# Kernel optimization log

Hardware: AMD Instinct MI355X
Metric: run time of the kernel (lower is better)

Reference implementation:

```python
import jax, jax.numpy as jnp
import numpy as np

N_NODES = 100000
N_EDGES = 3200000
IN_SIZE = 256
HID_SIZE = 256
OUT_SIZE = 64


def setup_inputs() -> dict:
    key = jax.random.key(0)
    ks = jax.random.split(key, 8)
    X = jax.random.normal(ks[0], (N_NODES, IN_SIZE), dtype=jnp.float32)
    edge_vals = jax.random.uniform(ks[1], (N_EDGES,), dtype=jnp.float32)
    # xavier-uniform-ish init for weights
    lim1 = float(np.sqrt(6.0 / (IN_SIZE + HID_SIZE)))
    W1 = jax.random.uniform(ks[2], (IN_SIZE, HID_SIZE), minval=-lim1, maxval=lim1, dtype=jnp.float32)
    b1 = jnp.zeros((HID_SIZE,), dtype=jnp.float32)
    lim2 = float(np.sqrt(6.0 / (HID_SIZE + OUT_SIZE)))
    W2 = jax.random.uniform(ks[3], (HID_SIZE, OUT_SIZE), minval=-lim2, maxval=lim2, dtype=jnp.float32)
    b2 = jnp.zeros((OUT_SIZE,), dtype=jnp.float32)
    row = jnp.sort(jax.random.randint(ks[4], (N_EDGES,), 0, N_NODES, dtype=jnp.int32))
    col = jax.random.randint(ks[5], (N_EDGES,), 0, N_NODES, dtype=jnp.int32)
    return {"X": X, "edge_vals": edge_vals, "W1": W1, "b1": b1,
            "W2": W2, "b2": b2, "row": row, "col": col}


def reference(X, edge_vals, W1, b1, W2, b2, row, col):
    """2-layer GCN (eval mode, dropout = identity).

    A is a sparse NxN matrix in COO form: A[row[e], col[e]] = edge_vals[e].
    Layer: relu(A @ (X @ W1) + b1); output: A @ (h @ W2) + b2.
    """
    n = X.shape[0]

    def spmm(dense):  # (A @ dense): gather columns, scale, segment-sum over rows
        gathered = edge_vals[:, None] * dense[col]        # [E, F]
        return jax.ops.segment_sum(gathered, row, num_segments=n)

    h = spmm(X @ W1) + b1          # [N, HID]
    h = jax.nn.relu(h)
    out = spmm(h @ W2) + b2        # [N, OUT]
    return out
```

## Files before the change

### kernel.cpp

```cpp
#include <hip/hip_runtime.h>


constexpr int IN_SIZE = 256;
constexpr int HID = 256;
constexpr int OUTF = 64;

typedef __bf16 bf16x8 __attribute__((ext_vector_type(8)));
typedef float f32x4 __attribute__((ext_vector_type(4)));

__device__ __forceinline__ ushort f2b(float f) {
    uint u = __float_as_uint(f);
    uint r = (u + 0x7fffu + ((u >> 16) & 1u)) >> 16;
    return (ushort)r;
}

__device__ __forceinline__ void fma4(float* a, uint word, float w) {
    a[0] += w * (float)(word & 0xffu);
    a[1] += w * (float)((word >> 8) & 0xffu);
    a[2] += w * (float)((word >> 16) & 0xffu);
    a[3] += w * (float)(word >> 24);
}

__device__ __forceinline__ bf16x8 pack8n(float4 a, float4 b) {
    bf16x8 h;
    h[0] = (__bf16)a.x; h[1] = (__bf16)a.y;
    h[2] = (__bf16)a.z; h[3] = (__bf16)a.w;
    h[4] = (__bf16)b.x; h[5] = (__bf16)b.y;
    h[6] = (__bf16)b.z; h[7] = (__bf16)b.w;
    return h;
}

__global__ void setup_kernel(const int* __restrict__ row, int* __restrict__ rp,
                             const float* __restrict__ W1, ushort* __restrict__ W1T,
                             const float* __restrict__ W2, ushort* __restrict__ W2T,
                             int n, int E, int rpB) {
    int b = blockIdx.x;
    if (b < rpB) {
        int i = b * 256 + threadIdx.x;
        if (i > n) return;
        int lo = 0, hi = E;
        while (lo < hi) {
            int mid = (lo + hi) >> 1;
            if (row[mid] < i) lo = mid + 1; else hi = mid;
        }
        rp[i] = lo;
    } else if (b < rpB + 256) {
        int nn = b - rpB;
        int k = threadIdx.x;
        W1T[(size_t)nn * 256 + k] = f2b(W1[(size_t)k * 256 + nn]);
    } else {
        int nn = b - rpB - 256;
        int k = threadIdx.x;
        W2T[(size_t)nn * 256 + k] = f2b(W2[(size_t)k * 64 + nn]);
    }
}

__global__ void prep_edges(const float* __restrict__ vals, const int* __restrict__ col,
                           const float* __restrict__ s, int2* __restrict__ ew,
                           int E, int shift) {
    int e = blockIdx.x * 256 + threadIdx.x;
    if (e >= E) return;
    int c = col[e];
    ew[e] = make_int2(c << shift, __float_as_int(vals[e] * s[c]));
}

__global__ __launch_bounds__(1024)
void gemm1_q(const float* __restrict__ A, const ushort* __restrict__ Bt,
             unsigned char* __restrict__ Q, float* __restrict__ s1, int M, int R) {
    __shared__ uint4 Wlds[8192];
    __shared__ float red[512];
    __shared__ float fin[256];
    const int tid = threadIdx.x;
    const int wave = tid >> 6, lane = tid & 63;
    const int quad = lane >> 4, l = lane & 15;
    const int wr = wave >> 1, wc = wave & 1;
    const int mstart = blockIdx.x * R;
    const int mend = min(mstart + R, M);

    for (int i = tid; i < 8192; i += 1024) {
        uint4 v = ((const uint4*)Bt)[i];
        Wlds[(i & ~31) | ((i & 31) ^ ((i >> 5) & 7))] = v;
    }
    __syncthreads();

    for (int m0 = mstart; m0 < mend; m0 += 256) {
        size_t abase[2];
#pragma unroll
        for (int mt = 0; mt < 2; ++mt) {
            int r = min(m0 + wr * 32 + mt * 16 + l, M - 1);
            abase[mt] = (size_t)r * 256 + quad * 8;
        }

        f32x4 acc[2][8] = {};
        float4 ra0[2], rb0[2], ra1[2], rb1[2];
#pragma unroll
        for (int mt = 0; mt < 2; ++mt) {
            ra0[mt] = *(const float4*)(A + abase[mt]);
            rb0[mt] = *(const float4*)(A + abase[mt] + 4);
            ra1[mt] = *(const float4*)(A + abase[mt] + 32);
            rb1[mt] = *(const float4*)(A + abase[mt] + 36);
        }

#pragma unroll
        for (int kstep = 0; kstep < 8; ++kstep) {
            bf16x8 af[2];
#pragma unroll
            for (int mt = 0; mt < 2; ++mt)
                af[mt] = pack8n(ra0[mt], rb0[mt]);
#pragma unroll
            for (int mt = 0; mt < 2; ++mt) { ra0[mt] = ra1[mt]; rb0[mt] = rb1[mt]; }
            if (kstep < 6) {
#pragma unroll
                for (int mt = 0; mt < 2; ++mt) {
                    ra1[mt] = *(const float4*)(A + abase[mt] + (kstep + 2) * 32);
                    rb1[mt] = *(const float4*)(A + abase[mt] + (kstep + 2) * 32 + 4);
                }
            }
#pragma unroll
            for (int nt = 0; nt < 8; ++nt) {
                int c = wc * 128 + nt * 16 + l;
                int idx = c * 32 + (((kstep << 2) + quad) ^ (c & 7));
                bf16x8 bfr = *(const bf16x8*)&Wlds[idx];
#pragma unroll
                for (int mt = 0; mt < 2; ++mt)
                    acc[mt][nt] = __builtin_amdgcn_mfma_f32_16x16x32_bf16(
                        af[mt], bfr, acc[mt][nt], 0, 0, 0);
            }
        }

        float rmax[2][4];
#pragma unroll
        for (int mt = 0; mt < 2; ++mt)
#pragma unroll
            for (int reg = 0; reg < 4; ++reg) {
                float m = 0.f;
#pragma unroll
                for (int nt = 0; nt < 8; ++nt)
                    m = fmaxf(m, fabsf(acc[mt][nt][reg]));
                rmax[mt][reg] = m;
            }
#pragma unroll
        for (int s = 1; s <= 8; s <<= 1)
#pragma unroll
            for (int mt = 0; mt < 2; ++mt)
#pragma unroll
                for (int reg = 0; reg < 4; ++reg)
                    rmax[mt][reg] = fmaxf(rmax[mt][reg], __shfl_xor(rmax[mt][reg], s));
        if (l < 4) {
#pragma unroll
            for (int mt = 0; mt < 2; ++mt)
                red[wc * 256 + wr * 32 + mt * 16 + quad * 4 + l] = rmax[mt][l];
        }
        __syncthreads();
        if (tid < 256) {
            float m = fmaxf(red[tid], red[256 + tid]);
            fin[tid] = m;
            int r = m0 + tid;
            if (r < mend) s1[r] = m * (1.f / 127.f);
        }
        __syncthreads();

#pragma unroll
        for (int mt = 0; mt < 2; ++mt)
#pragma unroll
            for (int reg = 0; reg < 4; ++reg) {
                int rl = wr * 32 + mt * 16 + quad * 4 + reg;
                int r = m0 + rl;
                if (r >= mend) continue;
                float m = fin[rl];
                float inv = m > 0.f ? 127.f / m : 0.f;
#pragma unroll
                for (int nt = 0; nt < 8; ++nt) {
                    int c = wc * 128 + nt * 16 + l;
                    Q[(size_t)r * 256 + c] =
                        (unsigned char)((int)rintf(acc[mt][nt][reg] * inv) + 128);
                }
            }
    }
}

__global__ __launch_bounds__(256, 4)
void gemm2_q(const ushort* __restrict__ A, const ushort* __restrict__ Bt,
             unsigned char* __restrict__ Q, float* __restrict__ s2, int M) {
    __shared__ uint4 Wlds[2048];
    const int tid = threadIdx.x;
    const int wave = tid >> 6, lane = tid & 63;
    const int quad = lane >> 4, l = lane & 15;
    const int r0 = blockIdx.x * 128 + wave * 32;

    for (int i = tid; i < 2048; i += 256) {
        uint4 v = ((const uint4*)Bt)[i];
        Wlds[(i & ~31) | ((i & 31) ^ ((i >> 5) & 7))] = v;
    }
    __syncthreads();

    size_t abase[2];
#pragma unroll
    for (int mt = 0; mt < 2; ++mt) {
        int r = min(r0 + mt * 16 + l, M - 1);
        abase[mt] = (size_t)r * 256 + quad * 8;
    }

    f32x4 acc[2][4] = {};
    uint4 ra0[2], ra1[2];
#pragma unroll
    for (int mt = 0; mt < 2; ++mt) {
        ra0[mt] = *(const uint4*)(A + abase[mt]);
        ra1[mt] = *(const uint4*)(A + abase[mt] + 32);
    }

#pragma unroll
    for (int kstep = 0; kstep < 8; ++kstep) {
        bf16x8 af[2];
#pragma unroll
        for (int mt = 0; mt < 2; ++mt)
            af[mt] = *(const bf16x8*)&ra0[mt];
#pragma unroll
        for (int mt = 0; mt < 2; ++mt) ra0[mt] = ra1[mt];
        if (kstep < 6) {
#pragma unroll
            for (int mt = 0; mt < 2; ++mt)
                ra1[mt] = *(const uint4*)(A + abase[mt] + (kstep + 2) * 32);
        }
        bf16x8 bfr[4];
#pragma unroll
        for (int nt = 0; nt < 4; ++nt) {
            int c = nt * 16 + l;
            int idx = c * 32 + (((kstep << 2) + quad) ^ (c & 7));
            bfr[nt] = *(const bf16x8*)&Wlds[idx];
        }
#pragma unroll
        for (int mt = 0; mt < 2; ++mt)
#pragma unroll
            for (int nt = 0; nt < 4; ++nt)
                acc[mt][nt] = __builtin_amdgcn_mfma_f32_16x16x32_bf16(
                    af[mt], bfr[nt], acc[mt][nt], 0, 0, 0);
    }

    float rmax[2][4];
#pragma unroll
    for (int mt = 0; mt < 2; ++mt)
#pragma unroll
        for (int reg = 0; reg < 4; ++reg) {
            float m = fmaxf(fabsf(acc[mt][0][reg]), fabsf(acc[mt][1][reg]));
            m = fmaxf(m, fabsf(acc[mt][2][reg]));
            m = fmaxf(m, fabsf(acc[mt][3][reg]));
            rmax[mt][reg] = m;
        }
#pragma unroll
    for (int s = 1; s <= 8; s <<= 1)
#pragma unroll
        for (int mt = 0; mt < 2; ++mt)
#pragma unroll
            for (int reg = 0; reg < 4; ++reg)
                rmax[mt][reg] = fmaxf(rmax[mt][reg], __shfl_xor(rmax[mt][reg], s));

#pragma unroll
    for (int mt = 0; mt < 2; ++mt)
#pragma unroll
        for (int reg = 0; reg < 4; ++reg) {
            int r = r0 + mt * 16 + quad * 4 + reg;
            if (r >= M) continue;
            float m = rmax[mt][reg];
            if (l == 0) s2[r] = m * (1.f / 127.f);
            float inv = m > 0.f ? 127.f / m : 0.f;
#pragma unroll
            for (int nt = 0; nt < 4; ++nt) {
                int c = nt * 16 + l;
                Q[(size_t)r * 64 + c] =
                    (unsigned char)((int)rintf(acc[mt][nt][reg] * inv) + 128);
            }
        }
}

__global__ __launch_bounds__(256)
void spmm1_q(const unsigned char* __restrict__ Q, const int2* __restrict__ ew,
             const int* __restrict__ rp, const float* __restrict__ bias,
             ushort* __restrict__ H, int node0, int nend) {
    const int wave = threadIdx.x >> 6;
    const int lane = threadIdx.x & 63;
    const int node = node0 + blockIdx.x * 4 + wave;
    if (node >= nend) return;
    const int e0 = rp[node], e1 = rp[node + 1];
    const int g = lane >> 4;
    const int fb = (lane & 15) * 16;

    float acc[16] = {};
    float sumw = 0.f;
    int e = e0;
    for (; e + 16 <= e1; e += 16) {
#pragma unroll
        for (int u = 0; u < 4; ++u) {
            int2 m = ew[e + u * 4 + g];
            float w = __int_as_float(m.y);
            uint4 qv = *(const uint4*)(Q + (size_t)(uint)m.x + fb);
            sumw += w;
            fma4(&acc[0], qv.x, w);
            fma4(&acc[4], qv.y, w);
            fma4(&acc[8], qv.z, w);
            fma4(&acc[12], qv.w, w);
        }
    }
    for (; e < e1; e += 4) {
        int idx = e + g;
        int2 m = ew[idx];
        bool ok = idx < e1;
        uint off = ok ? (uint)m.x : 0u;
        float w = ok ? __int_as_float(m.y) : 0.f;
        uint4 qv = *(const uint4*)(Q + (size_t)off + fb);
        sumw += w;
        fma4(&acc[0], qv.x, w);
        fma4(&acc[4], qv.y, w);
        fma4(&acc[8], qv.z, w);
        fma4(&acc[12], qv.w, w);
    }

#pragma unroll
    for (int s = 16; s <= 32; s <<= 1) {
#pragma unroll
        for (int j = 0; j < 16; ++j)
            acc[j] += __shfl_xor(acc[j], s);
        sumw += __shfl_xor(sumw, s);
    }

    if (g == 0) {
        const int f0 = (lane & 15) * 16;
        float4 b0 = *(const float4*)(bias + f0);
        float4 b1 = *(const float4*)(bias + f0 + 4);
        float4 b2 = *(const float4*)(bias + f0 + 8);
        float4 b3 = *(const float4*)(bias + f0 + 12);
        float bb[16] = {b0.x, b0.y, b0.z, b0.w, b1.x, b1.y, b1.z, b1.w,
                        b2.x, b2.y, b2.z, b2.w, b3.x, b3.y, b3.z, b3.w};
        float fix = -128.f * sumw;
        ushort r[16];
#pragma unroll
        for (int j = 0; j < 16; ++j)
            r[j] = f2b(fmaxf(acc[j] + fix + bb[j], 0.f));
        uint4 w0, w1;
        w0.x = (uint)r[0] | ((uint)r[1] << 16);
        w0.y = (uint)r[2] | ((uint)r[3] << 16);
        w0.z = (uint)r[4] | ((uint)r[5] << 16);
        w0.w = (uint)r[6] | ((uint)r[7] << 16);
        w1.x = (uint)r[8] | ((uint)r[9] << 16);
        w1.y = (uint)r[10] | ((uint)r[11] << 16);
        w1.z = (uint)r[12] | ((uint)r[13] << 16);
        w1.w = (uint)r[14] | ((uint)r[15] << 16);
        *(uint4*)(H + (size_t)node * 256 + f0) = w0;
        *(uint4*)(H + (size_t)node * 256 + f0 + 8) = w1;
    }
}

__global__ __launch_bounds__(256)
void spmm2_q(const unsigned char* __restrict__ Q, const int2* __restrict__ ew,
             const int* __restrict__ rp, const float* __restrict__ bias,
             float* __restrict__ O, int n) {
    const int wave = threadIdx.x >> 6;
    const int lane = threadIdx.x & 63;
    const int node = blockIdx.x * 4 + wave;
    if (node >= n) return;
    const int e0 = rp[node], e1 = rp[node + 1];
    const int g = lane >> 3;
    const int fb = (lane & 7) * 8;

    float acc[8] = {};
    float sumw = 0.f;
    int e = e0;
    for (; e + 16 <= e1; e += 16) {
#pragma unroll
        for (int u = 0; u < 2; ++u) {
            int2 m = ew[e + u * 8 + g];
            float w = __int_as_float(m.y);
            uint2 qv = *(const uint2*)(Q + (size_t)(uint)m.x + fb);
            sumw += w;
            fma4(&acc[0], qv.x, w);
            fma4(&acc[4], qv.y, w);
        }
    }
    for (; e < e1; e += 8) {
        int idx = e + g;
        int2 m = ew[idx];
        bool ok = idx < e1;
        uint off = ok ? (uint)m.x : 0u;
        float w = ok ? __int_as_float(m.y) : 0.f;
        uint2 qv = *(const uint2*)(Q + (size_t)off + fb);
        sumw += w;
        fma4(&acc[0], qv.x, w);
        fma4(&acc[4], qv.y, w);
    }

#pragma unroll
    for (int s = 8; s <= 32; s <<= 1) {
#pragma unroll
        for (int j = 0; j < 8; ++j)
            acc[j] += __shfl_xor(acc[j], s);
        sumw += __shfl_xor(sumw, s);
    }

    if (g == 0) {
        const int f0 = (lane & 7) * 8;
        float4 b0 = *(const float4*)(bias + f0);
        float4 b1 = *(const float4*)(bias + f0 + 4);
        float fix = -128.f * sumw;
        float4 o0, o1;
        o0.x = acc[0] + fix + b0.x;
        o0.y = acc[1] + fix + b0.y;
        o0.z = acc[2] + fix + b0.z;
        o0.w = acc[3] + fix + b0.w;
        o1.x = acc[4] + fix + b1.x;
        o1.y = acc[5] + fix + b1.y;
        o1.z = acc[6] + fix + b1.z;
        o1.w = acc[7] + fix + b1.w;
        *(float4*)(O + (size_t)node * 64 + f0) = o0;
        *(float4*)(O + (size_t)node * 64 + f0 + 4) = o1;
    }
}

static inline size_t alignup(size_t x) { return (x + 255) & ~(size_t)255; }

extern "C" void kernel_launch(void* const* d_in, const int* in_sizes, int n_in,
                              void* d_out, int out_size, void* d_ws, size_t ws_size,
                              hipStream_t stream) {
    const float* X  = (const float*)d_in[0];
    const float* ev = (const float*)d_in[1];
    const float* W1 = (const float*)d_in[2];
    const float* b1 = (const float*)d_in[3];
    const float* W2 = (const float*)d_in[4];
    const float* b2 = (const float*)d_in[5];
    const int*  row = (const int*)d_in[6];
    const int*  col = (const int*)d_in[7];
    float* out = (float*)d_out;

    const int n = in_sizes[0] / IN_SIZE;
    const int E = in_sizes[1];

    char* p = (char*)d_ws;
    ushort* H    = (ushort*)p; p += alignup((size_t)n * HID * 2);
    unsigned char* Q1 = (unsigned char*)p; p += alignup((size_t)n * HID);
    float*  s1   = (float*)p;  p += alignup((size_t)n * 4);
    unsigned char* Q2 = (unsigned char*)p; p += alignup((size_t)n * OUTF);
    float*  s2   = (float*)p;  p += alignup((size_t)n * 4);
    ushort* W1T  = (ushort*)p; p += alignup((size_t)IN_SIZE * HID * 2);
    ushort* W2T  = (ushort*)p; p += alignup((size_t)HID * OUTF * 2);
    int*    rp   = (int*)p;    p += alignup((size_t)(n + 1) * 4);
    int2*   ewb  = (int2*)p;   p += alignup((size_t)(E + 16) * 8);

    const int rpB = (n + 1 + 255) / 256;
    setup_kernel<<<rpB + 256 + 64, 256, 0, stream>>>(row, rp, W1, W1T, W2, W2T,
                                                     n, E, rpB);

    int R = ((n + 249) / 250 + 15) & ~15;
    int g1 = (n + R - 1) / R;
    gemm1_q<<<g1, 1024, 0, stream>>>(X, W1T, Q1, s1, n, R);

    prep_edges<<<(E + 255) / 256, 256, 0, stream>>>(ev, col, s1, ewb, E, 8);

    const int half = (n + 1) / 2;
    spmm1_q<<<(half + 3) / 4, 256, 0, stream>>>(Q1, ewb, rp, b1, H, 0, half);
    spmm1_q<<<(n - half + 3) / 4, 256, 0, stream>>>(Q1, ewb, rp, b1, H, half, n);

    gemm2_q<<<(n + 127) / 128, 256, 0, stream>>>(H, W2T, Q2, s2, n);

    prep_edges<<<(E + 255) / 256, 256, 0, stream>>>(ev, col, s2, ewb, E, 6);

    spmm2_q<<<(n + 3) / 4, 256, 0, stream>>>(Q2, ewb, rp, b2, out, n);
}
```

Baseline: 449.9 us.

## Prefetch next tile's A rows across iterations in gemm1 and split SpMM launches

The gemm1 A-operand loads become a three-slot register ring that, in the last k-steps, prefetches the first k-slices of the next 256-row tile, so the loop never stalls on global loads at tile boundaries. Layer-1 SpMM is split into four launches instead of two, and layer-2 SpMM into two, apparently to make each launch's gathered working set fit better in cache. The prefetch adds registers and loads clamped rows past the block's range, and the extra launches add launch overhead.

Measured after the change: 494.0 us. 9.8% more time.

```diff
diff --git a/kernel.cpp b/kernel.cpp
--- a/kernel.cpp
+++ b/kernel.cpp
@@ -83,37 +83,50 @@
     }
     __syncthreads();
 
+    size_t abase[2];
+#pragma unroll
+    for (int mt = 0; mt < 2; ++mt) {
+        int r = min(mstart + wr * 32 + mt * 16 + l, M - 1);
+        abase[mt] = (size_t)r * 256 + quad * 8;
+    }
+    float4 ra[3][2], rb[3][2];
+#pragma unroll
+    for (int kk = 0; kk < 3; ++kk)
+#pragma unroll
+        for (int mt = 0; mt < 2; ++mt) {
+            ra[kk][mt] = *(const float4*)(A + abase[mt] + kk * 32);
+            rb[kk][mt] = *(const float4*)(A + abase[mt] + kk * 32 + 4);
+        }
+
     for (int m0 = mstart; m0 < mend; m0 += 256) {
-        size_t abase[2];
+        size_t abaseN[2];
 #pragma unroll
         for (int mt = 0; mt < 2; ++mt) {
-            int r = min(m0 + wr * 32 + mt * 16 + l, M - 1);
-            abase[mt] = (size_t)r * 256 + quad * 8;
+            int r = min(min(m0 + 256, mend - 1) + wr * 32 + mt * 16 + l, M - 1);
+            abaseN[mt] = (size_t)r * 256 + quad * 8;
         }
 
         f32x4 acc[2][8] = {};
-        float4 ra0[2], rb0[2], ra1[2], rb1[2];
-#pragma unroll
-        for (int mt = 0; mt < 2; ++mt) {
-            ra0[mt] = *(const float4*)(A + abase[mt]);
-            rb0[mt] = *(const float4*)(A + abase[mt] + 4);
-            ra1[mt] = *(const float4*)(A + abase[mt] + 32);
-            rb1[mt] = *(const float4*)(A + abase[mt] + 36);
-        }
 
 #pragma unroll
         for (int kstep = 0; kstep < 8; ++kstep) {
+            const int slot = kstep % 3;
             bf16x8 af[2];
 #pragma unroll
             for (int mt = 0; mt < 2; ++mt)
-                af[mt] = pack8n(ra0[mt], rb0[mt]);
-#pragma unroll
-            for (int mt = 0; mt < 2; ++mt) { ra0[mt] = ra1[mt]; rb0[mt] = rb1[mt]; }
-            if (kstep < 6) {
+                af[mt] = pack8n(ra[slot][mt], rb[slot][mt]);
+            if (kstep < 5) {
 #pragma unroll
                 for (int mt = 0; mt < 2; ++mt) {
-                    ra1[mt] = *(const float4*)(A + abase[mt] + (kstep + 2) * 32);
-                    rb1[mt] = *(const float4*)(A + abase[mt] + (kstep + 2) * 32 + 4);
+                    ra[slot][mt] = *(const float4*)(A + abase[mt] + (kstep + 3) * 32);
+                    rb[slot][mt] = *(const float4*)(A + abase[mt] + (kstep + 3) * 32 + 4);
+                }
+            } else {
+                const int kn = kstep - 5;
+#pragma unroll
+                for (int mt = 0; mt < 2; ++mt) {
+                    ra[slot][mt] = *(const float4*)(A + abaseN[mt] + kn * 32);
+                    rb[slot][mt] = *(const float4*)(A + abaseN[mt] + kn * 32 + 4);
                 }
             }
 #pragma unroll
@@ -127,6 +140,15 @@
                         af[mt], bfr, acc[mt][nt], 0, 0, 0);
             }
         }
+        {
+            float4 t0, t1;
+#pragma unroll
+            for (int mt = 0; mt < 2; ++mt) {
+                t0 = ra[0][mt]; ra[0][mt] = ra[2][mt]; ra[2][mt] = ra[1][mt]; ra[1][mt] = t0;
+                t1 = rb[0][mt]; rb[0][mt] = rb[2][mt]; rb[2][mt] = rb[1][mt]; rb[1][mt] = t1;
+            }
+        }
+        abase[0] = abaseN[0]; abase[1] = abaseN[1];
 
         float rmax[2][4];
 #pragma unroll
@@ -353,11 +375,11 @@
 __global__ __launch_bounds__(256)
 void spmm2_q(const unsigned char* __restrict__ Q, const int2* __restrict__ ew,
              const int* __restrict__ rp, const float* __restrict__ bias,
-             float* __restrict__ O, int n) {
+             float* __restrict__ O, int node0, int nend) {
     const int wave = threadIdx.x >> 6;
     const int lane = threadIdx.x & 63;
-    const int node = blockIdx.x * 4 + wave;
-    if (node >= n) return;
+    const int node = node0 + blockIdx.x * 4 + wave;
+    if (node >= nend) return;
     const int e0 = rp[node], e1 = rp[node + 1];
     const int g = lane >> 3;
     const int fb = (lane & 7) * 8;
@@ -454,13 +476,20 @@
 
     prep_edges<<<(E + 255) / 256, 256, 0, stream>>>(ev, col, s1, ewb, E, 8);
 
+    const int nq = (n + 3) / 4;
+    for (int q = 0; q < 4; ++q) {
+        int node0 = q * nq;
+        int nend = min(n, node0 + nq);
+        if (node0 >= nend) break;
+        spmm1_q<<<(nend - node0 + 3) / 4, 256, 0, stream>>>(Q1, ewb, rp, b1, H,
+                                                            node0, nend);
+    }
+
+    gemm2_q<<<(n + 127) / 128, 256, 0, stream>>>(H, W2T, Q2, s2, n);
+
+    prep_edges<<<(E + 255) / 256, 256, 0, stream>>>(ev, col, s2, ewb, E, 6);
+
     const int half = (n + 1) / 2;
-    spmm1_q<<<(half + 3) / 4, 256, 0, stream>>>(Q1, ewb, rp, b1, H, 0, half);
-    spmm1_q<<<(n - half + 3) / 4, 256, 0, stream>>>(Q1, ewb, rp, b1, H, half, n);
-
-    gemm2_q<<<(n + 127) / 128, 256, 0, stream>>>(H, W2T, Q2, s2, n);
-
-    prep_edges<<<(E + 255) / 256, 256, 0, stream>>>(ev, col, s2, ewb, E, 6);
-
-    spmm2_q<<<(n + 3) / 4, 256, 0, stream>>>(Q2, ewb, rp, b2, out, n);
-}
+    spmm2_q<<<(half + 3) / 4, 256, 0, stream>>>(Q2, ewb, rp, b2, out, 0, half);
+    spmm2_q<<<(n - half + 3) / 4, 256, 0, stream>>>(Q2, ewb, rp, b2, out, half, n);
+}
```
